# Optimization experiments

Measured on AMD Instinct MI355X. Metric: run time of the kernel, lower is better.

Reference implementation:

```python
import jax, jax.numpy as jnp
import numpy as np

BN_EPS = 1e-5

def setup_inputs() -> dict:
    key = jax.random.key(0)
    k1, k2 = jax.random.split(key)
    B, C, H, W = 16, 256, 128, 128
    x = jax.random.normal(k1, (B, C, H, W), dtype=jnp.float32)
    w = jax.random.normal(k2, (C, 3), dtype=jnp.float32) * 0.1  # depthwise conv1d weight [c,1,3] squeezed
    gamma = jnp.ones((C,), dtype=jnp.float32)
    beta = jnp.zeros((C,), dtype=jnp.float32)
    running_mean = jnp.zeros((C,), dtype=jnp.float32)
    running_var = jnp.ones((C,), dtype=jnp.float32)
    return {"x": x, "w": w, "gamma": gamma, "beta": beta,
            "running_mean": running_mean, "running_var": running_var}


def reference(x, w, gamma, beta, running_mean, running_var):
    b, c, h, wd = x.shape
    xf = x.reshape(b, c, h * wd)
    mean = xf.mean(-1)                      # AdaptiveAvgPool2d(1)  -> [b,c]
    mx = xf.max(-1)                         # AdaptiveMaxPool2d(1)  -> [b,c]
    std = jnp.std(xf, axis=-1, ddof=1)      # torch std, unbiased   -> [b,c]
    u = jnp.stack([mean, mx, std], axis=-1)  # [b,c,3]
    # MS: per-batch median over the full [c,3] slice, then cube the deviation
    med = jnp.median(u.reshape(b, -1), axis=-1)  # [b]
    u = (u - med[:, None, None]) ** 3
    # depthwise Conv1d(k=3, groups=c) on length-3 input -> length-1 output
    z = jnp.einsum('bck,ck->bc', u, w)
    # BatchNorm1d (eval mode)
    z = (z - running_mean) * jax.lax.rsqrt(running_var + BN_EPS) * gamma + beta
    g = jax.nn.sigmoid(z)                    # [b,c]
    return x * g[:, :, None, None]
```

## Files before the change

### kernel.cpp

```cpp
#include <hip/hip_runtime.h>
#include <math.h>


typedef float fvec4 __attribute__((ext_vector_type(4)));

__global__ void stats_kernel(const float* __restrict__ x,
                             float* __restrict__ u, int HW) {
    const int bc  = blockIdx.x;
    const int tid = threadIdx.x;
    const float4* __restrict__ x4 =
        (const float4*)(x + (size_t)bc * (size_t)HW);
    const int n4 = HW >> 2;

    float s0 = 0.f, q0 = 0.f, m0 = -INFINITY;
    float s1 = 0.f, q1 = 0.f, m1 = -INFINITY;
    float s2 = 0.f, q2 = 0.f, m2 = -INFINITY;
    float s3 = 0.f, q3 = 0.f, m3 = -INFINITY;

    if (n4 == 4096) {
        #pragma unroll
        for (int k = 0; k < 4; ++k) {
            float4 a = x4[tid + (k * 4 + 0) * 256];
            float4 b = x4[tid + (k * 4 + 1) * 256];
            float4 c = x4[tid + (k * 4 + 2) * 256];
            float4 d = x4[tid + (k * 4 + 3) * 256];
            s0 += (a.x + a.y) + (a.z + a.w);
            q0 += (a.x * a.x + a.y * a.y) + (a.z * a.z + a.w * a.w);
            m0 = fmaxf(m0, fmaxf(fmaxf(a.x, a.y), fmaxf(a.z, a.w)));
            s1 += (b.x + b.y) + (b.z + b.w);
            q1 += (b.x * b.x + b.y * b.y) + (b.z * b.z + b.w * b.w);
            m1 = fmaxf(m1, fmaxf(fmaxf(b.x, b.y), fmaxf(b.z, b.w)));
            s2 += (c.x + c.y) + (c.z + c.w);
            q2 += (c.x * c.x + c.y * c.y) + (c.z * c.z + c.w * c.w);
            m2 = fmaxf(m2, fmaxf(fmaxf(c.x, c.y), fmaxf(c.z, c.w)));
            s3 += (d.x + d.y) + (d.z + d.w);
            q3 += (d.x * d.x + d.y * d.y) + (d.z * d.z + d.w * d.w);
            m3 = fmaxf(m3, fmaxf(fmaxf(d.x, d.y), fmaxf(d.z, d.w)));
        }
    } else {
        for (int i = tid; i < n4; i += 256) {
            float4 a = x4[i];
            s0 += (a.x + a.y) + (a.z + a.w);
            q0 += (a.x * a.x + a.y * a.y) + (a.z * a.z + a.w * a.w);
            m0 = fmaxf(m0, fmaxf(fmaxf(a.x, a.y), fmaxf(a.z, a.w)));
        }
    }
    float s = (s0 + s1) + (s2 + s3);
    float q = (q0 + q1) + (q2 + q3);
    float mx = fmaxf(fmaxf(m0, m1), fmaxf(m2, m3));

    for (int off = 32; off > 0; off >>= 1) {
        s  += __shfl_down(s, off);
        q  += __shfl_down(q, off);
        mx  = fmaxf(mx, __shfl_down(mx, off));
    }
    __shared__ float ss[4], sq[4], sm[4];
    const int wid = tid >> 6, lane = tid & 63;
    if (lane == 0) { ss[wid] = s; sq[wid] = q; sm[wid] = mx; }
    __syncthreads();
    if (tid == 0) {
        float S = ss[0] + ss[1] + ss[2] + ss[3];
        float Q = sq[0] + sq[1] + sq[2] + sq[3];
        float M = fmaxf(fmaxf(sm[0], sm[1]), fmaxf(sm[2], sm[3]));
        float mean = S / (float)HW;
        float var  = (Q - S * mean) / (float)(HW - 1);
        var = fmaxf(var, 0.f);
        float* up = u + (size_t)bc * 3;
        up[0] = mean;
        up[1] = M;
        up[2] = sqrtf(var);
    }
}

__global__ void median_gate_kernel(const float* __restrict__ u,
                                   const float* __restrict__ w,
                                   const float* __restrict__ gamma,
                                   const float* __restrict__ beta,
                                   const float* __restrict__ rmean,
                                   const float* __restrict__ rvar,
                                   float* __restrict__ g, int C) {
    const int b   = blockIdx.x;
    const int tid = threadIdx.x;
    const int NV  = C * 3;
    __shared__ float sv[768];
    __shared__ float ma, mb;

    const float* ub = u + (size_t)b * NV;
    for (int i = tid; i < NV; i += 256) sv[i] = ub[i];
    __syncthreads();

    float v0 = sv[tid], v1 = sv[tid + 256], v2 = sv[tid + 512];
    int lt0 = 0, eq0 = 0, lt1 = 0, eq1 = 0, lt2 = 0, eq2 = 0;
    for (int i = 0; i < NV; ++i) {
        float o = sv[i];
        lt0 += (o < v0); eq0 += (o == v0);
        lt1 += (o < v1); eq1 += (o == v1);
        lt2 += (o < v2); eq2 += (o == v2);
    }
    const int r0 = (NV - 1) / 2;
    const int r1 = NV / 2;
    if (lt0 <= r0 && r0 < lt0 + eq0) ma = v0;
    if (lt1 <= r0 && r0 < lt1 + eq1) ma = v1;
    if (lt2 <= r0 && r0 < lt2 + eq2) ma = v2;
    if (lt0 <= r1 && r1 < lt0 + eq0) mb = v0;
    if (lt1 <= r1 && r1 < lt1 + eq1) mb = v1;
    if (lt2 <= r1 && r1 < lt2 + eq2) mb = v2;
    __syncthreads();

    const float med = 0.5f * (ma + mb);
    if (tid < C) {
        const int c = tid;
        float z = 0.f;
        #pragma unroll
        for (int k = 0; k < 3; ++k) {
            float d = sv[c * 3 + k] - med;
            z += (d * d * d) * w[c * 3 + k];
        }
        z = (z - rmean[c]) * rsqrtf(rvar[c] + 1e-5f) * gamma[c] + beta[c];
        g[(size_t)b * C + c] = 1.f / (1.f + expf(-z));
    }
}

__global__ void scale_kernel(const float* __restrict__ x,
                             const float* __restrict__ g,
                             float* __restrict__ out, int HW) {
    const int bc = (int)gridDim.x - 1 - (int)blockIdx.x;
    const float gv = g[bc];
    const size_t base = (size_t)bc * (size_t)HW;
    const fvec4* __restrict__ x4 = (const fvec4*)(x + base);
    fvec4* __restrict__ o4 = (fvec4*)(out + base);
    const int n4 = HW >> 2;
    #pragma unroll 4
    for (int i = threadIdx.x; i < n4; i += 256) {
        fvec4 v = x4[i];
        v *= gv;
        __builtin_nontemporal_store(v, &o4[i]);
    }
}

extern "C" void kernel_launch(void* const* d_in, const int* in_sizes, int n_in,
                              void* d_out, int out_size, void* d_ws, size_t ws_size,
                              hipStream_t stream) {
    const float* x     = (const float*)d_in[0];
    const float* w     = (const float*)d_in[1];
    const float* gamma = (const float*)d_in[2];
    const float* beta  = (const float*)d_in[3];
    const float* rmean = (const float*)d_in[4];
    const float* rvar  = (const float*)d_in[5];
    float* out = (float*)d_out;

    const int C  = in_sizes[2];
    const int B  = 16;
    const int HW = in_sizes[0] / (B * C);

    float* u = (float*)d_ws;
    float* g = u + (size_t)B * C * 3;

    stats_kernel<<<B * C, 256, 0, stream>>>(x, u, HW);
    median_gate_kernel<<<B, 256, 0, stream>>>(u, w, gamma, beta, rmean, rvar, g, C);
    scale_kernel<<<B * C, 256, 0, stream>>>(x, g, out, HW);
}
```

Baseline: 161.8 us.

## Fuse median/gate into stats kernel via last-block atomic counter; tweak scale kernel

Merges the median and gate computation into the stats kernel. A per-batch atomic counter picks the last finishing block of each batch, and that block computes the median and gates, which removes one kernel launch and its serial tail. The scale kernel now walks blocks in forward order instead of reverse and uses non-temporal loads with an explicit 8-deep batch of loads. Forward order may lose L2 reuse of x data recently read by the stats pass. An extra memset launch is also added for the counters.

```diff
diff --git a/kernel.cpp b/kernel.cpp
--- a/kernel.cpp
+++ b/kernel.cpp
@@ -4,9 +4,18 @@
 
 typedef float fvec4 __attribute__((ext_vector_type(4)));
 
-__global__ void stats_kernel(const float* __restrict__ x,
-                             float* __restrict__ u, int HW) {
+__global__ void stats_median_kernel(const float* __restrict__ x,
+                                    const float* __restrict__ w,
+                                    const float* __restrict__ gamma,
+                                    const float* __restrict__ beta,
+                                    const float* __restrict__ rmean,
+                                    const float* __restrict__ rvar,
+                                    float* __restrict__ u,
+                                    float* __restrict__ g,
+                                    int* __restrict__ ctr,
+                                    int HW, int C) {
     const int bc  = blockIdx.x;
+    const int b   = bc / C;
     const int tid = threadIdx.x;
     const float4* __restrict__ x4 =
         (const float4*)(x + (size_t)bc * (size_t)HW);
@@ -21,15 +30,15 @@
         #pragma unroll
         for (int k = 0; k < 4; ++k) {
             float4 a = x4[tid + (k * 4 + 0) * 256];
-            float4 b = x4[tid + (k * 4 + 1) * 256];
+            float4 bb = x4[tid + (k * 4 + 1) * 256];
             float4 c = x4[tid + (k * 4 + 2) * 256];
             float4 d = x4[tid + (k * 4 + 3) * 256];
             s0 += (a.x + a.y) + (a.z + a.w);
             q0 += (a.x * a.x + a.y * a.y) + (a.z * a.z + a.w * a.w);
             m0 = fmaxf(m0, fmaxf(fmaxf(a.x, a.y), fmaxf(a.z, a.w)));
-            s1 += (b.x + b.y) + (b.z + b.w);
-            q1 += (b.x * b.x + b.y * b.y) + (b.z * b.z + b.w * b.w);
-            m1 = fmaxf(m1, fmaxf(fmaxf(b.x, b.y), fmaxf(b.z, b.w)));
+            s1 += (bb.x + bb.y) + (bb.z + bb.w);
+            q1 += (bb.x * bb.x + bb.y * bb.y) + (bb.z * bb.z + bb.w * bb.w);
+            m1 = fmaxf(m1, fmaxf(fmaxf(bb.x, bb.y), fmaxf(bb.z, bb.w)));
             s2 += (c.x + c.y) + (c.z + c.w);
             q2 += (c.x * c.x + c.y * c.y) + (c.z * c.z + c.w * c.w);
             m2 = fmaxf(m2, fmaxf(fmaxf(c.x, c.y), fmaxf(c.z, c.w)));
@@ -58,6 +67,8 @@
     const int wid = tid >> 6, lane = tid & 63;
     if (lane == 0) { ss[wid] = s; sq[wid] = q; sm[wid] = mx; }
     __syncthreads();
+
+    __shared__ int is_last;
     if (tid == 0) {
         float S = ss[0] + ss[1] + ss[2] + ss[3];
         float Q = sq[0] + sq[1] + sq[2] + sq[3];
@@ -69,22 +80,17 @@
         up[0] = mean;
         up[1] = M;
         up[2] = sqrtf(var);
+        __threadfence();
+        int old = __hip_atomic_fetch_add(&ctr[b], 1, __ATOMIC_ACQ_REL,
+                                         __HIP_MEMORY_SCOPE_AGENT);
+        is_last = (old == C - 1);
     }
-}
+    __syncthreads();
+    if (!is_last) return;
 
-__global__ void median_gate_kernel(const float* __restrict__ u,
-                                   const float* __restrict__ w,
-                                   const float* __restrict__ gamma,
-                                   const float* __restrict__ beta,
-                                   const float* __restrict__ rmean,
-                                   const float* __restrict__ rvar,
-                                   float* __restrict__ g, int C) {
-    const int b   = blockIdx.x;
-    const int tid = threadIdx.x;
-    const int NV  = C * 3;
+    const int NV = C * 3;
     __shared__ float sv[768];
     __shared__ float ma, mb;
-
     const float* ub = u + (size_t)b * NV;
     for (int i = tid; i < NV; i += 256) sv[i] = ub[i];
     __syncthreads();
@@ -124,17 +130,29 @@
 __global__ void scale_kernel(const float* __restrict__ x,
                              const float* __restrict__ g,
                              float* __restrict__ out, int HW) {
-    const int bc = (int)gridDim.x - 1 - (int)blockIdx.x;
+    const int bc = blockIdx.x;
     const float gv = g[bc];
     const size_t base = (size_t)bc * (size_t)HW;
     const fvec4* __restrict__ x4 = (const fvec4*)(x + base);
     fvec4* __restrict__ o4 = (fvec4*)(out + base);
     const int n4 = HW >> 2;
-    #pragma unroll 4
-    for (int i = threadIdx.x; i < n4; i += 256) {
-        fvec4 v = x4[i];
-        v *= gv;
-        __builtin_nontemporal_store(v, &o4[i]);
+    if (n4 == 4096) {
+        #pragma unroll
+        for (int half = 0; half < 2; ++half) {
+            const int bi = (int)threadIdx.x + half * 2048;
+            fvec4 r[8];
+            #pragma unroll
+            for (int k = 0; k < 8; ++k)
+                r[k] = __builtin_nontemporal_load(&x4[bi + k * 256]);
+            #pragma unroll
+            for (int k = 0; k < 8; ++k)
+                __builtin_nontemporal_store(r[k] * gv, &o4[bi + k * 256]);
+        }
+    } else {
+        for (int i = threadIdx.x; i < n4; i += 256) {
+            fvec4 v = __builtin_nontemporal_load(&x4[i]);
+            __builtin_nontemporal_store(v * gv, &o4[i]);
+        }
     }
 }
 
@@ -153,10 +171,13 @@
     const int B  = 16;
     const int HW = in_sizes[0] / (B * C);
 
-    float* u = (float*)d_ws;
-    float* g = u + (size_t)B * C * 3;
+    float* u   = (float*)d_ws;
+    float* g   = u + (size_t)B * C * 3;
+    int*   ctr = (int*)(g + (size_t)B * C);
 
-    stats_kernel<<<B * C, 256, 0, stream>>>(x, u, HW);
-    median_gate_kernel<<<B, 256, 0, stream>>>(u, w, gamma, beta, rmean, rvar, g, C);
+    hipMemsetAsync(ctr, 0, B * sizeof(int), stream);
+
+    stats_median_kernel<<<B * C, 256, 0, stream>>>(x, w, gamma, beta, rmean,
+                                                   rvar, u, g, ctr, HW, C);
     scale_kernel<<<B * C, 256, 0, stream>>>(x, g, out, HW);
 }
```

New measurement: 516.8 us. 219% more time.
